# Kernel tuning notes

Hardware: AMD Instinct MI355X
Metric: run time of the kernel (lower is better)

The kernel has to match this reference:

```python
import jax, jax.numpy as jnp
import numpy as np

N = 20000       # total atoms
E = 320000      # edges (avg degree 16)
F = 128         # num_features
R = 32          # num_radial
NB = 3          # num_blocks
CUTOFF = 5.0
MAX_Z = 37      # max_atomic_number + 1
MIN_DIST = 0.3
PI = 3.141592653589793


def swish(x):
    return x * jax.nn.sigmoid(x)


def sph_harm_l2(rhat):
    # Real spherical harmonics lmax=2, e3nn ordering, 'component' normalization.
    x, y, z = rhat[:, 0], rhat[:, 1], rhat[:, 2]
    s3, s5, s15 = 1.7320508075688772, 2.23606797749979, 3.872983346207417
    sh1 = jnp.stack([s3 * y, s3 * z, s3 * x], axis=-1)                    # l=1 (odd)
    sh2 = jnp.stack([s15 * x * y, s15 * y * z, 0.5 * s5 * (3.0 * z * z - 1.0),
                     s15 * z * x, 0.5 * s15 * (x * x - y * y)], axis=-1)  # l=2 (even)
    return sh1, sh2


def setup_inputs() -> dict:
    key = jax.random.key(0)
    ks = jax.random.split(key, 16)
    rn = lambda k, shape, scale: jax.random.normal(k, shape, dtype=jnp.float32) * scale
    inp = {}
    inp["z"] = jax.random.randint(ks[0], (N,), 0, MAX_Z)
    inp["pos"] = rn(ks[1], (N, 3), 3.0)
    inp["edge_index"] = jax.random.randint(ks[2], (2, E), 0, N)
    # embedding params
    inp["emb_table"] = rn(ks[3], (MAX_Z, F), 1.0)
    inp["emb_W"] = rn(ks[4], (F, F), F ** -0.5)
    inp["emb_b"] = jnp.zeros((F,), jnp.float32)
    # trainable Bessel frequencies (init n*pi, as in bessel RBF)
    inp["bessel_freq"] = jnp.arange(1, R + 1, dtype=jnp.float32) * PI
    # per-block params, stacked over NB blocks
    inp["Wf1"] = rn(ks[5], (NB, R, F), R ** -0.5)
    inp["bf1"] = jnp.zeros((NB, F), jnp.float32)
    inp["Wf2"] = rn(ks[6], (NB, F, 4 * F), F ** -0.5)
    inp["Wsrc"] = rn(ks[7], (NB, F, F), F ** -0.5)
    inp["Wu"] = rn(ks[8], (NB, F, 3 * F), F ** -0.5)
    inp["W1o"] = rn(ks[9], (NB, F, F), F ** -0.5)
    inp["W1e"] = rn(ks[10], (NB, F, F), F ** -0.5)
    inp["W2e"] = rn(ks[11], (NB, F, F), F ** -0.5)
    inp["Wup"] = rn(ks[12], (NB, 4 * F, F), (4 * F) ** -0.5)
    return inp


def forward(z, pos, edge_index, emb_table, emb_W, emb_b, bessel_freq,
            Wf1, bf1, Wf2, Wsrc, Wu, W1o, W1e, W2e, Wup):
    i, j = edge_index[0], edge_index[1]
    rij = pos[j] - pos[i]                                   # [E,3]
    r = jnp.sqrt(jnp.sum(rij * rij, axis=-1) + 1e-12)       # [E]
    rhat = rij / (r[:, None] + 1e-6)
    # mask replaces the edge filtering (min_distance and radius cutoff)
    edge_mask = ((r >= MIN_DIST) & (r < CUTOFF)).astype(pos.dtype)
    sh1, sh2 = sph_harm_l2(rhat)                            # [E,3], [E,5]
    # trainable Bessel RBF with cosine cutoff envelope
    fc = 0.5 * (jnp.cos(PI * r / CUTOFF) + 1.0) * edge_mask
    rbf = jnp.sqrt(2.0 / CUTOFF) * jnp.sin(bessel_freq[None, :] * r[:, None] / CUTOFF) / (r[:, None] + 1e-6)
    rbf = rbf * fc[:, None]                                 # [E,R]
    # atom embedding
    S = swish(emb_table[z] @ emb_W + emb_b)                 # [N,F]
    T = jnp.zeros((N, 11, F), S.dtype)                      # 1o(3)+1e(3)+2e(5) x F channels
    for b in range(NB):
        # radial filter network -> per-edge gates
        w = swish(rbf @ Wf1[b] + bf1[b]) @ Wf2[b]           # [E,4F]
        w = w * edge_mask[:, None]
        wS, w1, w2, w3 = jnp.split(w, 4, axis=-1)
        Sj = S[j]                                           # [E,F] gather
        # scalar messages
        mS = wS * swish(Sj @ Wsrc[b])                       # [E,F]
        aggS = jax.ops.segment_sum(mS, i, num_segments=N)   # [N,F]
        # equivariant messages: sh(l) outer-product edge features
        u1, u2, u3 = jnp.split(Sj @ Wu[b], 3, axis=-1)
        m1o = sh1[:, :, None] * (w1 * u1)[:, None, :]       # [E,3,F]
        m1e = sh1[:, :, None] * (w2 * u2)[:, None, :]       # [E,3,F]
        m2e = sh2[:, :, None] * (w3 * u3)[:, None, :]       # [E,5,F]
        mT = jnp.concatenate([m1o, m1e, m2e], axis=1)       # [E,11,F]
        aggT = jax.ops.segment_sum(mT, i, num_segments=N)   # [N,11,F] scatter-add
        Tin = T + aggT
        # per-irrep channel mixing (self-interaction)
        T1o = jnp.einsum('nmf,fg->nmg', Tin[:, 0:3], W1o[b])
        T1e = jnp.einsum('nmf,fg->nmg', Tin[:, 3:6], W1e[b])
        T2e = jnp.einsum('nmf,fg->nmg', Tin[:, 6:11], W2e[b])
        T = jnp.concatenate([T1o, T1e, T2e], axis=1)
        # invariant norms of each irrep feed back into scalar track
        inv = jnp.concatenate([jnp.sum(T1o * T1o, 1), jnp.sum(T1e * T1e, 1),
                               jnp.sum(T2e * T2e, 1)], axis=-1)   # [N,3F]
        S = S + swish(jnp.concatenate([aggS, inv], axis=-1) @ Wup[b])
    return S, T.reshape(N, 11 * F)


def reference(z, pos, edge_index, emb_table, emb_W, emb_b, bessel_freq,
              Wf1, bf1, Wf2, Wsrc, Wu, W1o, W1e, W2e, Wup):
    return forward(z, pos, edge_index, emb_table, emb_W, emb_b, bessel_freq,
                   Wf1, bf1, Wf2, Wsrc, Wu, W1o, W1e, W2e, Wup)
```

## Files before the change

kernel.cpp:

```cpp
#include <hip/hip_runtime.h>
#include <cstdint>
#include <cstddef>

#define NN 20000
#define EE 320000
#define FF 128
#define RR 32
#define MTE 16

typedef float  f32x4  __attribute__((ext_vector_type(4)));
typedef short  bf16x8 __attribute__((ext_vector_type(8)));

__device__ __forceinline__ float swishf(float x) {
    return x / (1.f + __expf(-x));
}
__device__ __forceinline__ unsigned short f2bf(float f) {
    unsigned int u = __builtin_bit_cast(unsigned int, f);
    u = (u + 0x7FFFu + ((u >> 16) & 1u)) >> 16;
    return (unsigned short)u;
}
__device__ __forceinline__ float bf2f(unsigned short h) {
    unsigned int u = ((unsigned int)h) << 16;
    return __builtin_bit_cast(float, u);
}

__global__ __launch_bounds__(256) void geom_deg_kernel(
    const float* __restrict__ pos, const int* __restrict__ eidx,
    int* __restrict__ deg)
{
    int e = blockIdx.x * 256 + threadIdx.x;
    if (e >= EE) return;
    int i = eidx[e], j = eidx[EE + e];
    float dx = pos[3*j+0] - pos[3*i+0];
    float dy = pos[3*j+1] - pos[3*i+1];
    float dz = pos[3*j+2] - pos[3*i+2];
    float r = sqrtf(dx*dx + dy*dy + dz*dz + 1e-12f);
    if (r >= 0.3f && r < 5.0f) atomicAdd(&deg[i], 1);
}

__global__ __launch_bounds__(256) void scan_kernel(
    const int* __restrict__ deg, int* __restrict__ cursor, int* __restrict__ cnt)
{
    __shared__ int part[256];
    const int t = threadIdx.x;
    const int lo = t * 79;
    const int hi = min(lo + 79, NN);
    int s = 0;
    for (int k = lo; k < hi; k++) s += deg[k];
    part[t] = s;
    __syncthreads();
    for (int off = 1; off < 256; off <<= 1) {
        int v = (t >= off) ? part[t - off] : 0;
        __syncthreads();
        part[t] += v;
        __syncthreads();
    }
    int run = (t == 0) ? 0 : part[t - 1];
    for (int k = lo; k < hi; k++) { cursor[k] = run; run += deg[k]; }
    if (t == 255) cnt[0] = part[255];
}

__global__ __launch_bounds__(256) void geom_scatter_kernel(
    const float* __restrict__ pos, const int* __restrict__ eidx,
    const float* __restrict__ freq, int* __restrict__ cursor,
    int* __restrict__ ei, int* __restrict__ ej,
    float* __restrict__ sh, unsigned short* __restrict__ rbfq)
{
    int e = blockIdx.x * 256 + threadIdx.x;
    if (e >= EE) return;
    int i = eidx[e], j = eidx[EE + e];
    float dx = pos[3*j+0] - pos[3*i+0];
    float dy = pos[3*j+1] - pos[3*i+1];
    float dz = pos[3*j+2] - pos[3*i+2];
    float r = sqrtf(dx*dx + dy*dy + dz*dz + 1e-12f);
    if (!(r >= 0.3f && r < 5.0f)) return;
    int slot = atomicAdd(&cursor[i], 1);
    ei[slot] = i; ej[slot] = j;
    float ir = 1.f / (r + 1e-6f);
    float x = dx*ir, y = dy*ir, z = dz*ir;
    const float s3 = 1.7320508075688772f, s5 = 2.23606797749979f, s15 = 3.872983346207417f;
    float* shp = sh + (size_t)slot * 8;
    shp[0] = s3*y; shp[1] = s3*z; shp[2] = s3*x;
    shp[3] = s15*x*y; shp[4] = s15*y*z; shp[5] = 0.5f*s5*(3.f*z*z - 1.f);
    shp[6] = s15*z*x; shp[7] = 0.5f*s15*(x*x - y*y);
    float fc = 0.5f * (cosf(3.14159265358979323846f * r * 0.2f) + 1.f);
    float pref = 0.6324555320336759f * fc * ir;
    unsigned short* rp = rbfq + (size_t)slot * RR;
    for (int k = 0; k < RR; k++) rp[k] = f2bf(pref * sinf(freq[k] * r * 0.2f));
}

__global__ __launch_bounds__(128) void embed_kernel(
    const int* __restrict__ z, const float* __restrict__ emb_table,
    const float* __restrict__ emb_W, const float* __restrict__ emb_b,
    float* __restrict__ S)
{
    int n = blockIdx.x;
    int f = threadIdx.x;
    __shared__ float row[FF];
    row[f] = emb_table[(size_t)z[n]*FF + f];
    __syncthreads();
    float acc = emb_b[f];
    for (int k = 0; k < FF; k++) acc += row[k] * emb_W[k*FF + f];
    S[(size_t)n*FF + f] = swishf(acc);
}

__global__ __launch_bounds__(256) void pack_kernel(
    const float* __restrict__ W1o, const float* __restrict__ W1e,
    const float* __restrict__ W2e, const float* __restrict__ Wup,
    unsigned short* __restrict__ ph, unsigned short* __restrict__ pl)
{
    int t = blockIdx.x * 256 + threadIdx.x;
    if (t >= 3 * 14336) return;
    int b = t / 14336, r = t % 14336;
    const float* src; int nks; size_t dstoff;
    if (r < 6144) {
        int mat = r / 2048, rr = r % 2048;
        src = (mat == 0 ? W1o : mat == 1 ? W1e : W2e) + (size_t)b * 16384;
        nks = 4;
        dstoff = (size_t)b * 114688 + (size_t)mat * 16384 + (size_t)rr * 8;
        r = rr;
    } else {
        int rr = r - 6144;
        src = Wup + (size_t)b * 65536;
        nks = 16;
        dstoff = (size_t)b * 114688 + 49152 + (size_t)rr * 8;
        r = rr;
    }
    int lane = r & 63;
    int fi = r >> 6;
    int ks = fi % nks, ct = fi / nks;
    int col = ct * 16 + (lane & 15);
    int kb = ks * 32 + (lane >> 4) * 8;
    #pragma unroll
    for (int e = 0; e < 8; e++) {
        float v = src[(size_t)(kb + e) * 128 + col];
        unsigned short h = f2bf(v);
        ph[dstoff + e] = h;
        pl[dstoff + e] = f2bf(v - bf2f(h));
    }
}

__global__ __launch_bounds__(256) void pack_pu_kernel(
    const float* __restrict__ Wsrc, const float* __restrict__ Wu,
    unsigned short* __restrict__ packPU)
{
    int t = blockIdx.x * 256 + threadIdx.x;
    if (t >= 3 * 8192) return;
    int b = t / 8192, r = t % 8192;
    int lane = r & 63, fi = r >> 6;
    int ks = fi & 3, ct = fi >> 2;
    int kb = ks * 32 + (lane >> 4) * 8;
    int colq = lane & 15;
    const float* src; int col, stride;
    if (ct < 8) { src = Wsrc + (size_t)b * 16384; col = ct*16 + colq; stride = 128; }
    else        { src = Wu   + (size_t)b * 49152; col = (ct-8)*16 + colq; stride = 384; }
    size_t dst = (size_t)b * 65536 + (size_t)fi * 512 + (size_t)lane * 8;
    #pragma unroll
    for (int e = 0; e < 8; e++)
        packPU[dst + e] = f2bf(src[(size_t)(kb + e) * stride + col]);
}

__global__ __launch_bounds__(256) void pack_f2_kernel(
    const float* __restrict__ Wf2, unsigned short* __restrict__ packF2)
{
    int t = blockIdx.x * 256 + threadIdx.x;
    if (t >= 3 * 8192) return;
    int b = t / 8192, r = t % 8192;
    int lane = r & 63, fi = r >> 6;
    int ks = fi & 3, ct = fi >> 2;
    int kb = ks * 32 + (lane >> 4) * 8;
    int col = ct * 16 + (lane & 15);
    const float* src = Wf2 + (size_t)b * 65536;
    size_t dst = (size_t)b * 65536 + (size_t)fi * 512 + (size_t)lane * 8;
    #pragma unroll
    for (int e = 0; e < 8; e++)
        packF2[dst + e] = f2bf(src[(size_t)(kb + e) * 512 + col]);
}

__global__ __launch_bounds__(256) void proj_kernel(
    const float* __restrict__ S, const unsigned short* __restrict__ packPU,
    unsigned short* __restrict__ PU)
{
    __shared__ float stage[16][132];
    const int tid = threadIdx.x;
    const int n0 = blockIdx.x * 16;

    for (int idx = tid; idx < 512; idx += 256) {
        int row = idx >> 5, k4 = (idx & 31) << 2;
        *(float4*)&stage[row][k4] = *(const float4*)&S[((size_t)(n0 + row) << 7) + k4];
    }
    __syncthreads();

    const int lane = tid & 63;
    const int wid  = tid >> 6;
    const int row  = lane & 15;
    const int k0   = (lane >> 4) * 8;

    f32x4 acc[8];
    #pragma unroll
    for (int c = 0; c < 8; c++) acc[c] = (f32x4){0.f, 0.f, 0.f, 0.f};

    #pragma unroll
    for (int ks = 0; ks < 4; ks++) {
        const float* sp = &stage[row][ks*32 + k0];
        bf16x8 a;
        #pragma unroll
        for (int e = 0; e < 8; e++) a[e] = (short)f2bf(sp[e]);
        #pragma unroll
        for (int cti = 0; cti < 8; cti++) {
            int ct = wid * 8 + cti;
            bf16x8 b = *(const bf16x8*)(packPU + (((size_t)ct * 4 + ks) * 64 + lane) * 8);
            acc[cti] = __builtin_amdgcn_mfma_f32_16x16x32_bf16(a, b, acc[cti], 0, 0, 0);
        }
    }

    #pragma unroll
    for (int cti = 0; cti < 8; cti++) {
        int ct = wid * 8 + cti;
        int col = ct * 16 + (lane & 15);
        #pragma unroll
        for (int q = 0; q < 4; q++) {
            int n = n0 + (lane >> 4) * 4 + q;
            float v = acc[cti][q];
            if (ct < 8) v = swishf(v);
            PU[(size_t)n * 512 + col] = f2bf(v);
        }
    }
}

__global__ __launch_bounds__(256) void msg_kernel(
    const int* __restrict__ cnt,
    const int* __restrict__ ei, const int* __restrict__ ej,
    const float* __restrict__ sh, const unsigned short* __restrict__ rbfq,
    const float* __restrict__ Wf1, const float* __restrict__ bf1,
    const unsigned short* __restrict__ packF2, const unsigned short* __restrict__ PU,
    float* __restrict__ aggS, float* __restrict__ aggT)
{
    const int Ea = cnt[0];
    const int base = blockIdx.x * MTE;
    if (base >= Ea) return;
    const int nval = min(MTE, Ea - base);
    const int tid = threadIdx.x;

    __shared__ float          rbf_s[MTE][RR];
    __shared__ unsigned short h_s[MTE][FF];
    __shared__ unsigned short w_s[MTE][512];
    __shared__ float          sh_s[MTE][8];
    __shared__ int            i_s[MTE];
    __shared__ int            j_s[MTE];

    if (tid < MTE) {
        i_s[tid] = (tid < nval) ? ei[base + tid] : -1;
        j_s[tid] = (tid < nval) ? ej[base + tid] : 0;
    }
    if (tid >= 64 && tid < 64 + MTE*8) {
        int t = tid - 64, e = t >> 3;
        sh_s[e][t & 7] = (e < nval) ? sh[(size_t)(base + e)*8 + (t & 7)] : 0.f;
    }
    for (int t = tid; t < MTE*RR; t += 256) {
        int e = t >> 5, k = t & 31;
        rbf_s[e][k] = (e < nval) ? bf2f(rbfq[(size_t)(base + e)*RR + k]) : 0.f;
    }
    __syncthreads();

    {
        const int f = tid & 127, eh = tid >> 7;
        float hacc[8];
        float bb = bf1[f];
        #pragma unroll
        for (int k = 0; k < 8; k++) hacc[k] = bb;
        for (int r = 0; r < RR; r++) {
            float wv = Wf1[r*FF + f];
            #pragma unroll
            for (int k = 0; k < 8; k++) hacc[k] += rbf_s[eh*8 + k][r] * wv;
        }
        #pragma unroll
        for (int k = 0; k < 8; k++) h_s[eh*8 + k][f] = f2bf(swishf(hacc[k]));
    }
    __syncthreads();

    {
        const int lane = tid & 63;
        const int wid  = tid >> 6;
        const int ra   = lane & 15;
        const int k0   = (lane >> 4) * 8;
        f32x4 acc[8];
        #pragma unroll
        for (int c = 0; c < 8; c++) acc[c] = (f32x4){0.f, 0.f, 0.f, 0.f};
        #pragma unroll
        for (int ks = 0; ks < 4; ks++) {
            bf16x8 a = *(const bf16x8*)&h_s[ra][ks*32 + k0];
            #pragma unroll
            for (int cti = 0; cti < 8; cti++) {
                int ct = wid * 8 + cti;
                bf16x8 b = *(const bf16x8*)(packF2 + (((size_t)ct * 4 + ks) * 64 + lane) * 8);
                acc[cti] = __builtin_amdgcn_mfma_f32_16x16x32_bf16(a, b, acc[cti], 0, 0, 0);
            }
        }
        #pragma unroll
        for (int cti = 0; cti < 8; cti++) {
            int ct = wid * 8 + cti;
            int col = ct * 16 + (lane & 15);
            #pragma unroll
            for (int q = 0; q < 4; q++)
                w_s[(lane >> 4)*4 + q][col] = f2bf(acc[cti][q]);
        }
    }
    __syncthreads();

    const int f = tid & 127;
    if (tid < 128) {
        float aS = 0.f, a3 = 0.f, a4 = 0.f, a5 = 0.f;
        int cur = i_s[0];
        for (int e = 0; e < nval; e++) {
            int ie = i_s[e];
            if (ie != cur) {
                atomicAdd(&aggS[((size_t)cur << 7) + f], aS);
                size_t bT = (((size_t)cur*11 + 3) << 7) + f;
                atomicAdd(&aggT[bT], a3); atomicAdd(&aggT[bT + 128], a4); atomicAdd(&aggT[bT + 256], a5);
                aS = a3 = a4 = a5 = 0.f; cur = ie;
            }
            const unsigned short* pu = PU + (size_t)j_s[e] * 512;
            float wS = bf2f(w_s[e][f]),       P  = bf2f(pu[f]);
            float w2 = bf2f(w_s[e][256 + f]), U2 = bf2f(pu[256 + f]);
            aS += wS * P;
            float v = w2 * U2;
            a3 += sh_s[e][0]*v; a4 += sh_s[e][1]*v; a5 += sh_s[e][2]*v;
        }
        atomicAdd(&aggS[((size_t)cur << 7) + f], aS);
        size_t bT = (((size_t)cur*11 + 3) << 7) + f;
        atomicAdd(&aggT[bT], a3); atomicAdd(&aggT[bT + 128], a4); atomicAdd(&aggT[bT + 256], a5);
    } else {
        float a0 = 0.f, a1 = 0.f, a2 = 0.f;
        float a6 = 0.f, a7 = 0.f, a8 = 0.f, a9 = 0.f, a10 = 0.f;
        int cur = i_s[0];
        for (int e = 0; e < nval; e++) {
            int ie = i_s[e];
            if (ie != cur) {
                size_t bT = (((size_t)cur*11) << 7) + f;
                atomicAdd(&aggT[bT], a0); atomicAdd(&aggT[bT + 128], a1); atomicAdd(&aggT[bT + 256], a2);
                size_t bT2 = (((size_t)cur*11 + 6) << 7) + f;
                atomicAdd(&aggT[bT2], a6); atomicAdd(&aggT[bT2 + 128], a7); atomicAdd(&aggT[bT2 + 256], a8);
                atomicAdd(&aggT[bT2 + 384], a9); atomicAdd(&aggT[bT2 + 512], a10);
                a0 = a1 = a2 = a6 = a7 = a8 = a9 = a10 = 0.f; cur = ie;
            }
            const unsigned short* pu = PU + (size_t)j_s[e] * 512;
            float w1 = bf2f(w_s[e][128 + f]), U1 = bf2f(pu[128 + f]);
            float w3 = bf2f(w_s[e][384 + f]), U3 = bf2f(pu[384 + f]);
            float v1 = w1 * U1;
            a0 += sh_s[e][0]*v1; a1 += sh_s[e][1]*v1; a2 += sh_s[e][2]*v1;
            float v3 = w3 * U3;
            a6 += sh_s[e][3]*v3; a7 += sh_s[e][4]*v3; a8 += sh_s[e][5]*v3;
            a9 += sh_s[e][6]*v3; a10 += sh_s[e][7]*v3;
        }
        size_t bT = (((size_t)cur*11) << 7) + f;
        atomicAdd(&aggT[bT], a0); atomicAdd(&aggT[bT + 128], a1); atomicAdd(&aggT[bT + 256], a2);
        size_t bT2 = (((size_t)cur*11 + 6) << 7) + f;
        atomicAdd(&aggT[bT2], a6); atomicAdd(&aggT[bT2 + 128], a7); atomicAdd(&aggT[bT2 + 256], a8);
        atomicAdd(&aggT[bT2 + 384], a9); atomicAdd(&aggT[bT2 + 512], a10);
    }
}

template<int GSIZE>
__global__ __launch_bounds__(256) void tgemm_kernel(
    const float* __restrict__ aggT,
    const unsigned short* __restrict__ Wh, const unsigned short* __restrict__ Wl,
    float* __restrict__ T, float* __restrict__ inv,
    int goff, int invoff, int addT)
{
    __shared__ float stage[GSIZE][16][132];
    const int tid = threadIdx.x;
    const int n0 = blockIdx.x * 16;

    const int total = GSIZE * 16 * 32;
    for (int idx = tid; idx < total; idx += 256) {
        int mg  = idx >> 9;
        int rem = idx & 511;
        int row = rem >> 5;
        int k4  = (rem & 31) << 2;
        size_t g = (((size_t)(n0 + row) * 11 + goff + mg) << 7) + k4;
        float4 v = *(const float4*)&aggT[g];
        if (addT) {
            float4 tv = *(const float4*)&T[g];
            v.x += tv.x; v.y += tv.y; v.z += tv.z; v.w += tv.w;
        }
        *(float4*)&stage[mg][row][k4] = v;
    }
    __syncthreads();

    const int lane = tid & 63;
    const int wid  = tid >> 6;
    const int row  = lane & 15;
    const int k0   = (lane >> 4) * 8;

    f32x4 acc[GSIZE][2];
    #pragma unroll
    for (int mg = 0; mg < GSIZE; mg++) {
        acc[mg][0] = (f32x4){0.f, 0.f, 0.f, 0.f};
        acc[mg][1] = (f32x4){0.f, 0.f, 0.f, 0.f};
    }

    #pragma unroll
    for (int ks = 0; ks < 4; ks++) {
        bf16x8 ah[GSIZE], al[GSIZE];
        #pragma unroll
        for (int mg = 0; mg < GSIZE; mg++) {
            const float* sp = &stage[mg][row][ks*32 + k0];
            float v0[4], v1[4];
            *(float4*)v0 = *(const float4*)sp;
            *(float4*)v1 = *(const float4*)(sp + 4);
            #pragma unroll
            for (int e = 0; e < 4; e++) {
                unsigned short h0 = f2bf(v0[e]);
                ah[mg][e]   = (short)h0;
                al[mg][e]   = (short)f2bf(v0[e] - bf2f(h0));
                unsigned short h1 = f2bf(v1[e]);
                ah[mg][4+e] = (short)h1;
                al[mg][4+e] = (short)f2bf(v1[e] - bf2f(h1));
            }
        }
        #pragma unroll
        for (int cti = 0; cti < 2; cti++) {
            const int ct = wid * 2 + cti;
            size_t boff = (((size_t)ct * 4 + ks) * 64 + lane) * 8;
            bf16x8 bh = *(const bf16x8*)(Wh + boff);
            bf16x8 bl = *(const bf16x8*)(Wl + boff);
            #pragma unroll
            for (int mg = 0; mg < GSIZE; mg++) {
                acc[mg][cti] = __builtin_amdgcn_mfma_f32_16x16x32_bf16(ah[mg], bh, acc[mg][cti], 0, 0, 0);
                acc[mg][cti] = __builtin_amdgcn_mfma_f32_16x16x32_bf16(al[mg], bh, acc[mg][cti], 0, 0, 0);
                acc[mg][cti] = __builtin_amdgcn_mfma_f32_16x16x32_bf16(ah[mg], bl, acc[mg][cti], 0, 0, 0);
            }
        }
    }

    #pragma unroll
    for (int cti = 0; cti < 2; cti++) {
        const int ct = wid * 2 + cti;
        const int fc = ct * 16 + (lane & 15);
        #pragma unroll
        for (int q = 0; q < 4; q++) {
            const int n = n0 + (lane >> 4) * 4 + q;
            float iv = 0.f;
            #pragma unroll
            for (int mg = 0; mg < GSIZE; mg++) {
                float o = acc[mg][cti][q];
                T[(((size_t)n * 11 + goff + mg) << 7) + fc] = o;
                iv += o * o;
            }
            inv[(size_t)n * 384 + invoff + fc] = iv;
        }
    }
}

__global__ __launch_bounds__(256) void sgemm2_kernel(
    const float* __restrict__ aggS, const float* __restrict__ inv,
    const unsigned short* __restrict__ Wh, const unsigned short* __restrict__ Wl,
    float* __restrict__ S)
{
    __shared__ float stage[16][516];
    const int tid = threadIdx.x;
    const int n0 = blockIdx.x * 16;

    for (int idx = tid; idx < 16 * 128; idx += 256) {
        int row = idx >> 7;
        int k4  = (idx & 127) << 2;
        float4 v;
        if (k4 < 128) v = *(const float4*)&aggS[((size_t)(n0 + row) << 7) + k4];
        else          v = *(const float4*)&inv[(size_t)(n0 + row) * 384 + (k4 - 128)];
        *(float4*)&stage[row][k4] = v;
    }
    __syncthreads();

    const int lane = tid & 63;
    const int wid  = tid >> 6;
    const int row  = lane & 15;
    const int k0   = (lane >> 4) * 8;

    f32x4 acc[2];
    acc[0] = (f32x4){0.f, 0.f, 0.f, 0.f};
    acc[1] = (f32x4){0.f, 0.f, 0.f, 0.f};

    for (int ks = 0; ks < 16; ks++) {
        const float* sp = &stage[row][ks*32 + k0];
        float v0[4], v1[4];
        *(float4*)v0 = *(const float4*)sp;
        *(float4*)v1 = *(const float4*)(sp + 4);
        bf16x8 ah, al;
        #pragma unroll
        for (int e = 0; e < 4; e++) {
            unsigned short h0 = f2bf(v0[e]);
            ah[e]   = (short)h0;
            al[e]   = (short)f2bf(v0[e] - bf2f(h0));
            unsigned short h1 = f2bf(v1[e]);
            ah[4+e] = (short)h1;
            al[4+e] = (short)f2bf(v1[e] - bf2f(h1));
        }
        #pragma unroll
        for (int cti = 0; cti < 2; cti++) {
            const int ct = wid * 2 + cti;
            size_t boff = (((size_t)ct * 16 + ks) * 64 + lane) * 8;
            bf16x8 bh = *(const bf16x8*)(Wh + boff);
            bf16x8 bl = *(const bf16x8*)(Wl + boff);
            acc[cti] = __builtin_amdgcn_mfma_f32_16x16x32_bf16(ah, bh, acc[cti], 0, 0, 0);
            acc[cti] = __builtin_amdgcn_mfma_f32_16x16x32_bf16(al, bh, acc[cti], 0, 0, 0);
            acc[cti] = __builtin_amdgcn_mfma_f32_16x16x32_bf16(ah, bl, acc[cti], 0, 0, 0);
        }
    }

    #pragma unroll
    for (int cti = 0; cti < 2; cti++) {
        const int ct = wid * 2 + cti;
        const int fc = ct * 16 + (lane & 15);
        #pragma unroll
        for (int q = 0; q < 4; q++) {
            const int n = n0 + (lane >> 4) * 4 + q;
            size_t o = ((size_t)n << 7) + fc;
            S[o] += swishf(acc[cti][q]);
        }
    }
}

extern "C" void kernel_launch(void* const* d_in, const int* in_sizes, int n_in,
                              void* d_out, int out_size, void* d_ws, size_t ws_size,
                              hipStream_t stream)
{
    const int*   z         = (const int*)  d_in[0];
    const float* pos       = (const float*)d_in[1];
    const int*   eidx      = (const int*)  d_in[2];
    const float* emb_table = (const float*)d_in[3];
    const float* emb_W     = (const float*)d_in[4];
    const float* emb_b     = (const float*)d_in[5];
    const float* freq      = (const float*)d_in[6];
    const float* Wf1       = (const float*)d_in[7];
    const float* bf1       = (const float*)d_in[8];
    const float* Wf2       = (const float*)d_in[9];
    const float* Wsrc      = (const float*)d_in[10];
    const float* Wu        = (const float*)d_in[11];
    const float* W1o       = (const float*)d_in[12];
    const float* W1e       = (const float*)d_in[13];
    const float* W2e       = (const float*)d_in[14];
    const float* Wup       = (const float*)d_in[15];

    float* S = (float*)d_out;
    float* T = S + (size_t)NN*FF;

    char* w = (char*)d_ws;
    int*   cnt    = (int*)w;                      w += 256;
    int*   deg    = (int*)w;                      w += (size_t)NN*4 + 128;
    int*   cursor = (int*)w;                      w += (size_t)NN*4 + 128;
    int*   ei     = (int*)w;                      w += (size_t)EE*4;
    int*   ej     = (int*)w;                      w += (size_t)EE*4;
    float* sh     = (float*)w;                    w += (size_t)EE*8*4;
    unsigned short* rbfq = (unsigned short*)w;    w += (size_t)EE*RR*2;
    unsigned short* PU   = (unsigned short*)w;    w += (size_t)NN*512*2;
    float* aggS   = (float*)w;                    w += (size_t)NN*FF*4;
    float* aggT   = (float*)w;                    w += (size_t)NN*11*FF*4;
    float* inv    = (float*)w;                    w += (size_t)NN*384*4;
    unsigned short* packH  = (unsigned short*)w;  w += (size_t)344064*2;
    unsigned short* packL  = (unsigned short*)w;  w += (size_t)344064*2;
    unsigned short* packPU = (unsigned short*)w;  w += (size_t)3*65536*2;
    unsigned short* packF2 = (unsigned short*)w;  w += (size_t)3*65536*2;

    hipMemsetAsync(deg, 0, (size_t)NN*4, stream);

    geom_deg_kernel<<<(EE + 255)/256, 256, 0, stream>>>(pos, eidx, deg);
    scan_kernel<<<1, 256, 0, stream>>>(deg, cursor, cnt);
    geom_scatter_kernel<<<(EE + 255)/256, 256, 0, stream>>>(pos, eidx, freq, cursor, ei, ej, sh, rbfq);
    embed_kernel<<<NN, 128, 0, stream>>>(z, emb_table, emb_W, emb_b, S);
    pack_kernel<<<(3*14336 + 255)/256, 256, 0, stream>>>(W1o, W1e, W2e, Wup, packH, packL);
    pack_pu_kernel<<<(3*8192 + 255)/256, 256, 0, stream>>>(Wsrc, Wu, packPU);
    pack_f2_kernel<<<(3*8192 + 255)/256, 256, 0, stream>>>(Wf2, packF2);

    for (int b = 0; b < 3; b++) {
        hipMemsetAsync(aggS, 0, (size_t)NN*FF*4 + (size_t)NN*11*FF*4, stream);
        proj_kernel<<<NN/16, 256, 0, stream>>>(S, packPU + (size_t)b*65536, PU);
        msg_kernel<<<(EE + MTE - 1)/MTE, 256, 0, stream>>>(
            cnt, ei, ej, sh, rbfq,
            Wf1 + (size_t)b*RR*FF, bf1 + (size_t)b*FF,
            packF2 + (size_t)b*65536, PU, aggS, aggT);

        const unsigned short* H = packH + (size_t)b*114688;
        const unsigned short* L = packL + (size_t)b*114688;
        tgemm_kernel<3><<<NN/16, 256, 0, stream>>>(aggT, H +     0, L +     0, T, inv, 0,   0, b > 0);
        tgemm_kernel<3><<<NN/16, 256, 0, stream>>>(aggT, H + 16384, L + 16384, T, inv, 3, 128, b > 0);
        tgemm_kernel<5><<<NN/16, 256, 0, stream>>>(aggT, H + 32768, L + 32768, T, inv, 6, 256, b > 0);
        sgemm2_kernel<<<NN/16, 256, 0, stream>>>(aggS, inv, H + 49152, L + 49152, S);
    }
}
```

Measured before the change: 985.2 us.

## Fuse message passing, aggregation and node GEMMs into one per-node-block kernel

Replaces the per-layer message kernel, global atomic aggregation, memset and four node GEMM kernels with a single kernel. Each block owns 8 destination nodes, walks their CSR edge range, and accumulates messages in LDS without atomics. It then applies the T and S channel-mixing GEMMs directly from LDS. PU and the per-edge filter weights are interleaved so one 8-byte load fetches all four channels per feature. This drops the global aggT/aggS/inv round-trips and the atomics, but the 16-row MFMA tiles now carry only 8 valid rows, and degree imbalance between blocks may cause load imbalance.

Result: slower. 2.164 ms (+119.6%).

```diff
diff --git a/kernel.cpp b/kernel.cpp
--- a/kernel.cpp
+++ b/kernel.cpp
@@ -6,7 +6,7 @@
 #define EE 320000
 #define FF 128
 #define RR 32
-#define MTE 16
+#define NB_NODES 8
 
 typedef float  f32x4  __attribute__((ext_vector_type(4)));
 typedef short  bf16x8 __attribute__((ext_vector_type(8)));
@@ -39,7 +39,7 @@
 }
 
 __global__ __launch_bounds__(256) void scan_kernel(
-    const int* __restrict__ deg, int* __restrict__ cursor, int* __restrict__ cnt)
+    const int* __restrict__ deg, int* __restrict__ cursor, int* __restrict__ cstart)
 {
     __shared__ int part[256];
     const int t = threadIdx.x;
@@ -56,8 +56,8 @@
         __syncthreads();
     }
     int run = (t == 0) ? 0 : part[t - 1];
-    for (int k = lo; k < hi; k++) { cursor[k] = run; run += deg[k]; }
-    if (t == 255) cnt[0] = part[255];
+    for (int k = lo; k < hi; k++) { cursor[k] = run; cstart[k] = run; run += deg[k]; }
+    if (t == 255) cstart[NN] = run;
 }
 
 __global__ __launch_bounds__(256) void geom_scatter_kernel(
@@ -217,306 +217,308 @@
     #pragma unroll
     for (int cti = 0; cti < 8; cti++) {
         int ct = wid * 8 + cti;
-        int col = ct * 16 + (lane & 15);
+        int cblk = ct >> 3;
+        int fcol = (ct & 7) * 16 + (lane & 15);
         #pragma unroll
         for (int q = 0; q < 4; q++) {
             int n = n0 + (lane >> 4) * 4 + q;
             float v = acc[cti][q];
-            if (ct < 8) v = swishf(v);
-            PU[(size_t)n * 512 + col] = f2bf(v);
-        }
-    }
-}
-
-__global__ __launch_bounds__(256) void msg_kernel(
-    const int* __restrict__ cnt,
+            if (cblk == 0) v = swishf(v);
+            PU[(size_t)n * 512 + fcol * 4 + cblk] = f2bf(v);
+        }
+    }
+}
+
+template<int GS>
+__device__ __forceinline__ void tgemm_group(
+    const float* aggT_lds, float* inv_lds,
+    const unsigned short* __restrict__ Hb, const unsigned short* __restrict__ Lb,
+    float* __restrict__ T, int n0, int goff, int invoff, int lane, int wid)
+{
+    const int arow = lane & 15;
+    const int k0 = (lane >> 4) * 8;
+    f32x4 acc[GS][2];
+    #pragma unroll
+    for (int mg = 0; mg < GS; mg++) {
+        acc[mg][0] = (f32x4){0.f, 0.f, 0.f, 0.f};
+        acc[mg][1] = (f32x4){0.f, 0.f, 0.f, 0.f};
+    }
+    #pragma unroll
+    for (int ks = 0; ks < 4; ks++) {
+        bf16x8 ah[GS], al[GS];
+        #pragma unroll
+        for (int mg = 0; mg < GS; mg++) {
+            float v[8];
+            if (arow < NB_NODES) {
+                const float* sp = aggT_lds + arow*1452 + (goff+mg)*132 + ks*32 + k0;
+                *(float4*)&v[0] = *(const float4*)sp;
+                *(float4*)&v[4] = *(const float4*)(sp + 4);
+            } else {
+                #pragma unroll
+                for (int e = 0; e < 8; e++) v[e] = 0.f;
+            }
+            #pragma unroll
+            for (int e = 0; e < 8; e++) {
+                unsigned short h = f2bf(v[e]);
+                ah[mg][e] = (short)h;
+                al[mg][e] = (short)f2bf(v[e] - bf2f(h));
+            }
+        }
+        #pragma unroll
+        for (int cti = 0; cti < 2; cti++) {
+            int ct = wid * 2 + cti;
+            size_t boff = (((size_t)ct * 4 + ks) * 64 + lane) * 8;
+            bf16x8 bh = *(const bf16x8*)(Hb + boff);
+            bf16x8 bl = *(const bf16x8*)(Lb + boff);
+            #pragma unroll
+            for (int mg = 0; mg < GS; mg++) {
+                acc[mg][cti] = __builtin_amdgcn_mfma_f32_16x16x32_bf16(ah[mg], bh, acc[mg][cti], 0, 0, 0);
+                acc[mg][cti] = __builtin_amdgcn_mfma_f32_16x16x32_bf16(al[mg], bh, acc[mg][cti], 0, 0, 0);
+                acc[mg][cti] = __builtin_amdgcn_mfma_f32_16x16x32_bf16(ah[mg], bl, acc[mg][cti], 0, 0, 0);
+            }
+        }
+    }
+    #pragma unroll
+    for (int cti = 0; cti < 2; cti++) {
+        int ct = wid * 2 + cti;
+        int fc = ct * 16 + (lane & 15);
+        #pragma unroll
+        for (int q = 0; q < 4; q++) {
+            int rowD = (lane >> 4) * 4 + q;
+            if (rowD < NB_NODES) {
+                float iv = 0.f;
+                #pragma unroll
+                for (int mg = 0; mg < GS; mg++) {
+                    float o = acc[mg][cti][q];
+                    T[(((size_t)(n0+rowD)*11 + goff + mg) << 7) + fc] = o;
+                    iv += o * o;
+                }
+                inv_lds[rowD*388 + invoff + fc] = iv;
+            }
+        }
+    }
+}
+
+__global__ __launch_bounds__(256, 2) void fused_layer_kernel(
+    const int* __restrict__ cstart,
     const int* __restrict__ ei, const int* __restrict__ ej,
     const float* __restrict__ sh, const unsigned short* __restrict__ rbfq,
     const float* __restrict__ Wf1, const float* __restrict__ bf1,
     const unsigned short* __restrict__ packF2, const unsigned short* __restrict__ PU,
-    float* __restrict__ aggS, float* __restrict__ aggT)
-{
-    const int Ea = cnt[0];
-    const int base = blockIdx.x * MTE;
-    if (base >= Ea) return;
-    const int nval = min(MTE, Ea - base);
+    const unsigned short* __restrict__ packH, const unsigned short* __restrict__ packL,
+    float* __restrict__ S, float* __restrict__ T, int addT)
+{
+    __shared__ float aggT_lds[NB_NODES * 1452];
+    __shared__ float aggS_lds[NB_NODES * 132];
+    __shared__ unsigned short upool[16 * 520];
+    __shared__ unsigned short h_s[16][128];
+    __shared__ float rbf_s[16][32];
+    __shared__ float sh_s[16][8];
+    __shared__ int   i_s[16], j_s[16];
+
     const int tid = threadIdx.x;
-
-    __shared__ float          rbf_s[MTE][RR];
-    __shared__ unsigned short h_s[MTE][FF];
-    __shared__ unsigned short w_s[MTE][512];
-    __shared__ float          sh_s[MTE][8];
-    __shared__ int            i_s[MTE];
-    __shared__ int            j_s[MTE];
-
-    if (tid < MTE) {
-        i_s[tid] = (tid < nval) ? ei[base + tid] : -1;
-        j_s[tid] = (tid < nval) ? ej[base + tid] : 0;
-    }
-    if (tid >= 64 && tid < 64 + MTE*8) {
-        int t = tid - 64, e = t >> 3;
-        sh_s[e][t & 7] = (e < nval) ? sh[(size_t)(base + e)*8 + (t & 7)] : 0.f;
-    }
-    for (int t = tid; t < MTE*RR; t += 256) {
-        int e = t >> 5, k = t & 31;
-        rbf_s[e][k] = (e < nval) ? bf2f(rbfq[(size_t)(base + e)*RR + k]) : 0.f;
-    }
-    __syncthreads();
-
-    {
-        const int f = tid & 127, eh = tid >> 7;
-        float hacc[8];
-        float bb = bf1[f];
-        #pragma unroll
-        for (int k = 0; k < 8; k++) hacc[k] = bb;
-        for (int r = 0; r < RR; r++) {
-            float wv = Wf1[r*FF + f];
-            #pragma unroll
-            for (int k = 0; k < 8; k++) hacc[k] += rbf_s[eh*8 + k][r] * wv;
-        }
-        #pragma unroll
-        for (int k = 0; k < 8; k++) h_s[eh*8 + k][f] = f2bf(swishf(hacc[k]));
-    }
-    __syncthreads();
-
-    {
-        const int lane = tid & 63;
-        const int wid  = tid >> 6;
-        const int ra   = lane & 15;
-        const int k0   = (lane >> 4) * 8;
-        f32x4 acc[8];
-        #pragma unroll
-        for (int c = 0; c < 8; c++) acc[c] = (f32x4){0.f, 0.f, 0.f, 0.f};
-        #pragma unroll
-        for (int ks = 0; ks < 4; ks++) {
-            bf16x8 a = *(const bf16x8*)&h_s[ra][ks*32 + k0];
+    const int n0 = blockIdx.x * NB_NODES;
+    const int estart = cstart[n0];
+    const int eend   = cstart[n0 + NB_NODES];
+    const int f    = tid & 127;
+    const int half = tid >> 7;
+    const int lane = tid & 63;
+    const int wid  = tid >> 6;
+
+    for (int k = tid; k < NB_NODES*1452; k += 256) aggT_lds[k] = 0.f;
+    for (int k = tid; k < NB_NODES*132; k += 256)  aggS_lds[k] = 0.f;
+
+    float aS=0.f, a3=0.f, a4=0.f, a5=0.f;
+    float a0=0.f,a1=0.f,a2=0.f,a6=0.f,a7=0.f,a8=0.f,a9=0.f,a10=0.f;
+    int cur = -1;
+
+    for (int eoff = estart; eoff < eend; eoff += 16) {
+        const int te = min(16, eend - eoff);
+        __syncthreads();
+        if (tid < 16) {
+            i_s[tid] = (tid < te) ? ei[eoff + tid] : -1;
+            j_s[tid] = (tid < te) ? ej[eoff + tid] : 0;
+        }
+        if (tid >= 64 && tid < 192) {
+            int t = tid - 64, e = t >> 3;
+            sh_s[e][t & 7] = (e < te) ? sh[(size_t)(eoff + e)*8 + (t & 7)] : 0.f;
+        }
+        for (int t = tid; t < 512; t += 256) {
+            int e = t >> 5, k = t & 31;
+            rbf_s[e][k] = (e < te) ? bf2f(rbfq[(size_t)(eoff + e)*RR + k]) : 0.f;
+        }
+        __syncthreads();
+        if (cur < 0) cur = i_s[0];
+
+        uint2 puv[16];
+        #pragma unroll
+        for (int e = 0; e < 16; e++)
+            puv[e] = *(const uint2*)(PU + ((size_t)j_s[e] << 9) + (f << 2));
+
+        {
+            float hacc[8];
+            float bb = bf1[f];
+            #pragma unroll
+            for (int k = 0; k < 8; k++) hacc[k] = bb;
+            for (int r = 0; r < RR; r++) {
+                float wv = Wf1[r*FF + f];
+                #pragma unroll
+                for (int k = 0; k < 8; k++) hacc[k] += rbf_s[half*8 + k][r] * wv;
+            }
+            #pragma unroll
+            for (int k = 0; k < 8; k++)
+                h_s[half*8 + k][f] = (half*8 + k < te) ? f2bf(swishf(hacc[k])) : 0;
+        }
+        __syncthreads();
+
+        {
+            const int ra = lane & 15, k0 = (lane >> 4) * 8;
+            f32x4 wacc[8];
+            #pragma unroll
+            for (int c = 0; c < 8; c++) wacc[c] = (f32x4){0.f, 0.f, 0.f, 0.f};
+            #pragma unroll
+            for (int ks = 0; ks < 4; ks++) {
+                bf16x8 a = *(const bf16x8*)&h_s[ra][ks*32 + k0];
+                #pragma unroll
+                for (int cti = 0; cti < 8; cti++) {
+                    int ct = wid * 8 + cti;
+                    bf16x8 b = *(const bf16x8*)(packF2 + (((size_t)ct * 4 + ks) * 64 + lane) * 8);
+                    wacc[cti] = __builtin_amdgcn_mfma_f32_16x16x32_bf16(a, b, wacc[cti], 0, 0, 0);
+                }
+            }
             #pragma unroll
             for (int cti = 0; cti < 8; cti++) {
                 int ct = wid * 8 + cti;
-                bf16x8 b = *(const bf16x8*)(packF2 + (((size_t)ct * 4 + ks) * 64 + lane) * 8);
-                acc[cti] = __builtin_amdgcn_mfma_f32_16x16x32_bf16(a, b, acc[cti], 0, 0, 0);
-            }
-        }
-        #pragma unroll
-        for (int cti = 0; cti < 8; cti++) {
-            int ct = wid * 8 + cti;
-            int col = ct * 16 + (lane & 15);
-            #pragma unroll
-            for (int q = 0; q < 4; q++)
-                w_s[(lane >> 4)*4 + q][col] = f2bf(acc[cti][q]);
+                int cblk = ct >> 3;
+                int fcol = (ct & 7) * 16 + (lane & 15);
+                #pragma unroll
+                for (int q = 0; q < 4; q++)
+                    upool[((lane >> 4)*4 + q)*520 + fcol*4 + cblk] = f2bf(wacc[cti][q]);
+            }
+        }
+        __syncthreads();
+
+        #pragma unroll
+        for (int e = 0; e < 16; e++) {
+            bool valid = (e < te);
+            int ie = valid ? i_s[e] : cur;
+            if (ie != cur) {
+                int ln = cur - n0;
+                float* base = aggT_lds + ln*1452;
+                if (half == 0) {
+                    aggS_lds[ln*132 + f] = aS;
+                    base[3*132+f] = a3; base[4*132+f] = a4; base[5*132+f] = a5;
+                    aS = a3 = a4 = a5 = 0.f;
+                } else {
+                    base[f] = a0; base[132+f] = a1; base[264+f] = a2;
+                    base[6*132+f] = a6; base[7*132+f] = a7; base[8*132+f] = a8;
+                    base[9*132+f] = a9; base[10*132+f] = a10;
+                    a0=a1=a2=a6=a7=a8=a9=a10=0.f;
+                }
+                cur = ie;
+            }
+            uint2 wv2 = *(const uint2*)&upool[e*520 + f*4];
+            uint2 pv  = puv[e];
+            if (half == 0) {
+                float wS = bf2f((unsigned short)(wv2.x & 0xffff));
+                float w2 = bf2f((unsigned short)(wv2.y & 0xffff));
+                float P  = bf2f((unsigned short)(pv.x  & 0xffff));
+                float U2 = bf2f((unsigned short)(pv.y  & 0xffff));
+                aS += wS * P;
+                float v = w2 * U2;
+                a3 += sh_s[e][0]*v; a4 += sh_s[e][1]*v; a5 += sh_s[e][2]*v;
+            } else {
+                float w1 = bf2f((unsigned short)(wv2.x >> 16));
+                float w3 = bf2f((unsigned short)(wv2.y >> 16));
+                float U1 = bf2f((unsigned short)(pv.x  >> 16));
+                float U3 = bf2f((unsigned short)(pv.y  >> 16));
+                float v1 = w1 * U1;
+                a0 += sh_s[e][0]*v1; a1 += sh_s[e][1]*v1; a2 += sh_s[e][2]*v1;
+                float v3 = w3 * U3;
+                a6 += sh_s[e][3]*v3; a7 += sh_s[e][4]*v3; a8 += sh_s[e][5]*v3;
+                a9 += sh_s[e][6]*v3; a10 += sh_s[e][7]*v3;
+            }
+        }
+    }
+    if (eend > estart) {
+        int ln = cur - n0;
+        float* base = aggT_lds + ln*1452;
+        if (half == 0) {
+            aggS_lds[ln*132 + f] = aS;
+            base[3*132+f] = a3; base[4*132+f] = a4; base[5*132+f] = a5;
+        } else {
+            base[f] = a0; base[132+f] = a1; base[264+f] = a2;
+            base[6*132+f] = a6; base[7*132+f] = a7; base[8*132+f] = a8;
+            base[9*132+f] = a9; base[10*132+f] = a10;
         }
     }
     __syncthreads();
 
-    const int f = tid & 127;
-    if (tid < 128) {
-        float aS = 0.f, a3 = 0.f, a4 = 0.f, a5 = 0.f;
-        int cur = i_s[0];
-        for (int e = 0; e < nval; e++) {
-            int ie = i_s[e];
-            if (ie != cur) {
-                atomicAdd(&aggS[((size_t)cur << 7) + f], aS);
-                size_t bT = (((size_t)cur*11 + 3) << 7) + f;
-                atomicAdd(&aggT[bT], a3); atomicAdd(&aggT[bT + 128], a4); atomicAdd(&aggT[bT + 256], a5);
-                aS = a3 = a4 = a5 = 0.f; cur = ie;
-            }
-            const unsigned short* pu = PU + (size_t)j_s[e] * 512;
-            float wS = bf2f(w_s[e][f]),       P  = bf2f(pu[f]);
-            float w2 = bf2f(w_s[e][256 + f]), U2 = bf2f(pu[256 + f]);
-            aS += wS * P;
-            float v = w2 * U2;
-            a3 += sh_s[e][0]*v; a4 += sh_s[e][1]*v; a5 += sh_s[e][2]*v;
-        }
-        atomicAdd(&aggS[((size_t)cur << 7) + f], aS);
-        size_t bT = (((size_t)cur*11 + 3) << 7) + f;
-        atomicAdd(&aggT[bT], a3); atomicAdd(&aggT[bT + 128], a4); atomicAdd(&aggT[bT + 256], a5);
-    } else {
-        float a0 = 0.f, a1 = 0.f, a2 = 0.f;
-        float a6 = 0.f, a7 = 0.f, a8 = 0.f, a9 = 0.f, a10 = 0.f;
-        int cur = i_s[0];
-        for (int e = 0; e < nval; e++) {
-            int ie = i_s[e];
-            if (ie != cur) {
-                size_t bT = (((size_t)cur*11) << 7) + f;
-                atomicAdd(&aggT[bT], a0); atomicAdd(&aggT[bT + 128], a1); atomicAdd(&aggT[bT + 256], a2);
-                size_t bT2 = (((size_t)cur*11 + 6) << 7) + f;
-                atomicAdd(&aggT[bT2], a6); atomicAdd(&aggT[bT2 + 128], a7); atomicAdd(&aggT[bT2 + 256], a8);
-                atomicAdd(&aggT[bT2 + 384], a9); atomicAdd(&aggT[bT2 + 512], a10);
-                a0 = a1 = a2 = a6 = a7 = a8 = a9 = a10 = 0.f; cur = ie;
-            }
-            const unsigned short* pu = PU + (size_t)j_s[e] * 512;
-            float w1 = bf2f(w_s[e][128 + f]), U1 = bf2f(pu[128 + f]);
-            float w3 = bf2f(w_s[e][384 + f]), U3 = bf2f(pu[384 + f]);
-            float v1 = w1 * U1;
-            a0 += sh_s[e][0]*v1; a1 += sh_s[e][1]*v1; a2 += sh_s[e][2]*v1;
-            float v3 = w3 * U3;
-            a6 += sh_s[e][3]*v3; a7 += sh_s[e][4]*v3; a8 += sh_s[e][5]*v3;
-            a9 += sh_s[e][6]*v3; a10 += sh_s[e][7]*v3;
-        }
-        size_t bT = (((size_t)cur*11) << 7) + f;
-        atomicAdd(&aggT[bT], a0); atomicAdd(&aggT[bT + 128], a1); atomicAdd(&aggT[bT + 256], a2);
-        size_t bT2 = (((size_t)cur*11 + 6) << 7) + f;
-        atomicAdd(&aggT[bT2], a6); atomicAdd(&aggT[bT2 + 128], a7); atomicAdd(&aggT[bT2 + 256], a8);
-        atomicAdd(&aggT[bT2 + 384], a9); atomicAdd(&aggT[bT2 + 512], a10);
-    }
-}
-
-template<int GSIZE>
-__global__ __launch_bounds__(256) void tgemm_kernel(
-    const float* __restrict__ aggT,
-    const unsigned short* __restrict__ Wh, const unsigned short* __restrict__ Wl,
-    float* __restrict__ T, float* __restrict__ inv,
-    int goff, int invoff, int addT)
-{
-    __shared__ float stage[GSIZE][16][132];
-    const int tid = threadIdx.x;
-    const int n0 = blockIdx.x * 16;
-
-    const int total = GSIZE * 16 * 32;
-    for (int idx = tid; idx < total; idx += 256) {
-        int mg  = idx >> 9;
-        int rem = idx & 511;
-        int row = rem >> 5;
-        int k4  = (rem & 31) << 2;
-        size_t g = (((size_t)(n0 + row) * 11 + goff + mg) << 7) + k4;
-        float4 v = *(const float4*)&aggT[g];
-        if (addT) {
-            float4 tv = *(const float4*)&T[g];
-            v.x += tv.x; v.y += tv.y; v.z += tv.z; v.w += tv.w;
-        }
-        *(float4*)&stage[mg][row][k4] = v;
+    if (addT) {
+        for (int idx = tid; idx < NB_NODES*11*32; idx += 256) {
+            int node = idx / 352;
+            int rem  = idx % 352;
+            int m = rem >> 5, k4 = (rem & 31) << 2;
+            float4 tv = *(const float4*)&T[(((size_t)(n0 + node)*11 + m) << 7) + k4];
+            float* dst = &aggT_lds[node*1452 + m*132 + k4];
+            dst[0] += tv.x; dst[1] += tv.y; dst[2] += tv.z; dst[3] += tv.w;
+        }
     }
     __syncthreads();
 
-    const int lane = tid & 63;
-    const int wid  = tid >> 6;
-    const int row  = lane & 15;
-    const int k0   = (lane >> 4) * 8;
-
-    f32x4 acc[GSIZE][2];
-    #pragma unroll
-    for (int mg = 0; mg < GSIZE; mg++) {
-        acc[mg][0] = (f32x4){0.f, 0.f, 0.f, 0.f};
-        acc[mg][1] = (f32x4){0.f, 0.f, 0.f, 0.f};
-    }
-
-    #pragma unroll
-    for (int ks = 0; ks < 4; ks++) {
-        bf16x8 ah[GSIZE], al[GSIZE];
-        #pragma unroll
-        for (int mg = 0; mg < GSIZE; mg++) {
-            const float* sp = &stage[mg][row][ks*32 + k0];
-            float v0[4], v1[4];
-            *(float4*)v0 = *(const float4*)sp;
-            *(float4*)v1 = *(const float4*)(sp + 4);
-            #pragma unroll
-            for (int e = 0; e < 4; e++) {
-                unsigned short h0 = f2bf(v0[e]);
-                ah[mg][e]   = (short)h0;
-                al[mg][e]   = (short)f2bf(v0[e] - bf2f(h0));
-                unsigned short h1 = f2bf(v1[e]);
-                ah[mg][4+e] = (short)h1;
-                al[mg][4+e] = (short)f2bf(v1[e] - bf2f(h1));
+    float* inv_lds = (float*)upool;
+    tgemm_group<3>(aggT_lds, inv_lds, packH +     0, packL +     0, T, n0, 0,   0, lane, wid);
+    tgemm_group<3>(aggT_lds, inv_lds, packH + 16384, packL + 16384, T, n0, 3, 128, lane, wid);
+    tgemm_group<5>(aggT_lds, inv_lds, packH + 32768, packL + 32768, T, n0, 6, 256, lane, wid);
+    __syncthreads();
+
+    {
+        const int arow = lane & 15;
+        const int k0 = (lane >> 4) * 8;
+        f32x4 acc[2];
+        acc[0] = (f32x4){0.f, 0.f, 0.f, 0.f};
+        acc[1] = (f32x4){0.f, 0.f, 0.f, 0.f};
+        #pragma unroll
+        for (int ks = 0; ks < 16; ks++) {
+            float v[8];
+            #pragma unroll
+            for (int e = 0; e < 8; e++) {
+                int kk = ks*32 + k0 + e;
+                float x = 0.f;
+                if (arow < NB_NODES)
+                    x = (kk < 128) ? aggS_lds[arow*132 + kk] : inv_lds[arow*388 + (kk - 128)];
+                v[e] = x;
+            }
+            bf16x8 ah, al;
+            #pragma unroll
+            for (int e = 0; e < 8; e++) {
+                unsigned short h = f2bf(v[e]);
+                ah[e] = (short)h;
+                al[e] = (short)f2bf(v[e] - bf2f(h));
+            }
+            #pragma unroll
+            for (int cti = 0; cti < 2; cti++) {
+                int ct = wid * 2 + cti;
+                size_t boff = (((size_t)ct * 16 + ks) * 64 + lane) * 8 + 49152;
+                bf16x8 bh = *(const bf16x8*)(packH + boff);
+                bf16x8 bl = *(const bf16x8*)(packL + boff);
+                acc[cti] = __builtin_amdgcn_mfma_f32_16x16x32_bf16(ah, bh, acc[cti], 0, 0, 0);
+                acc[cti] = __builtin_amdgcn_mfma_f32_16x16x32_bf16(al, bh, acc[cti], 0, 0, 0);
+                acc[cti] = __builtin_amdgcn_mfma_f32_16x16x32_bf16(ah, bl, acc[cti], 0, 0, 0);
             }
         }
         #pragma unroll
         for (int cti = 0; cti < 2; cti++) {
-            const int ct = wid * 2 + cti;
-            size_t boff = (((size_t)ct * 4 + ks) * 64 + lane) * 8;
-            bf16x8 bh = *(const bf16x8*)(Wh + boff);
-            bf16x8 bl = *(const bf16x8*)(Wl + boff);
-            #pragma unroll
-            for (int mg = 0; mg < GSIZE; mg++) {
-                acc[mg][cti] = __builtin_amdgcn_mfma_f32_16x16x32_bf16(ah[mg], bh, acc[mg][cti], 0, 0, 0);
-                acc[mg][cti] = __builtin_amdgcn_mfma_f32_16x16x32_bf16(al[mg], bh, acc[mg][cti], 0, 0, 0);
-                acc[mg][cti] = __builtin_amdgcn_mfma_f32_16x16x32_bf16(ah[mg], bl, acc[mg][cti], 0, 0, 0);
-            }
-        }
-    }
-
-    #pragma unroll
-    for (int cti = 0; cti < 2; cti++) {
-        const int ct = wid * 2 + cti;
-        const int fc = ct * 16 + (lane & 15);
-        #pragma unroll
-        for (int q = 0; q < 4; q++) {
-            const int n = n0 + (lane >> 4) * 4 + q;
-            float iv = 0.f;
-            #pragma unroll
-            for (int mg = 0; mg < GSIZE; mg++) {
-                float o = acc[mg][cti][q];
-                T[(((size_t)n * 11 + goff + mg) << 7) + fc] = o;
-                iv += o * o;
-            }
-            inv[(size_t)n * 384 + invoff + fc] = iv;
-        }
-    }
-}
-
-__global__ __launch_bounds__(256) void sgemm2_kernel(
-    const float* __restrict__ aggS, const float* __restrict__ inv,
-    const unsigned short* __restrict__ Wh, const unsigned short* __restrict__ Wl,
-    float* __restrict__ S)
-{
-    __shared__ float stage[16][516];
-    const int tid = threadIdx.x;
-    const int n0 = blockIdx.x * 16;
-
-    for (int idx = tid; idx < 16 * 128; idx += 256) {
-        int row = idx >> 7;
-        int k4  = (idx & 127) << 2;
-        float4 v;
-        if (k4 < 128) v = *(const float4*)&aggS[((size_t)(n0 + row) << 7) + k4];
-        else          v = *(const float4*)&inv[(size_t)(n0 + row) * 384 + (k4 - 128)];
-        *(float4*)&stage[row][k4] = v;
-    }
-    __syncthreads();
-
-    const int lane = tid & 63;
-    const int wid  = tid >> 6;
-    const int row  = lane & 15;
-    const int k0   = (lane >> 4) * 8;
-
-    f32x4 acc[2];
-    acc[0] = (f32x4){0.f, 0.f, 0.f, 0.f};
-    acc[1] = (f32x4){0.f, 0.f, 0.f, 0.f};
-
-    for (int ks = 0; ks < 16; ks++) {
-        const float* sp = &stage[row][ks*32 + k0];
-        float v0[4], v1[4];
-        *(float4*)v0 = *(const float4*)sp;
-        *(float4*)v1 = *(const float4*)(sp + 4);
-        bf16x8 ah, al;
-        #pragma unroll
-        for (int e = 0; e < 4; e++) {
-            unsigned short h0 = f2bf(v0[e]);
-            ah[e]   = (short)h0;
-            al[e]   = (short)f2bf(v0[e] - bf2f(h0));
-            unsigned short h1 = f2bf(v1[e]);
-            ah[4+e] = (short)h1;
-            al[4+e] = (short)f2bf(v1[e] - bf2f(h1));
-        }
-        #pragma unroll
-        for (int cti = 0; cti < 2; cti++) {
-            const int ct = wid * 2 + cti;
-            size_t boff = (((size_t)ct * 16 + ks) * 64 + lane) * 8;
-            bf16x8 bh = *(const bf16x8*)(Wh + boff);
-            bf16x8 bl = *(const bf16x8*)(Wl + boff);
-            acc[cti] = __builtin_amdgcn_mfma_f32_16x16x32_bf16(ah, bh, acc[cti], 0, 0, 0);
-            acc[cti] = __builtin_amdgcn_mfma_f32_16x16x32_bf16(al, bh, acc[cti], 0, 0, 0);
-            acc[cti] = __builtin_amdgcn_mfma_f32_16x16x32_bf16(ah, bl, acc[cti], 0, 0, 0);
-        }
-    }
-
-    #pragma unroll
-    for (int cti = 0; cti < 2; cti++) {
-        const int ct = wid * 2 + cti;
-        const int fc = ct * 16 + (lane & 15);
-        #pragma unroll
-        for (int q = 0; q < 4; q++) {
-            const int n = n0 + (lane >> 4) * 4 + q;
-            size_t o = ((size_t)n << 7) + fc;
-            S[o] += swishf(acc[cti][q]);
+            int ct = wid * 2 + cti;
+            int fc = ct * 16 + (lane & 15);
+            #pragma unroll
+            for (int q = 0; q < 4; q++) {
+                int rowD = (lane >> 4) * 4 + q;
+                if (rowD < NB_NODES) {
+                    size_t o = ((size_t)(n0 + rowD) << 7) + fc;
+                    S[o] += swishf(acc[cti][q]);
+                }
+            }
         }
     }
 }
@@ -546,17 +548,14 @@
     float* T = S + (size_t)NN*FF;
 
     char* w = (char*)d_ws;
-    int*   cnt    = (int*)w;                      w += 256;
     int*   deg    = (int*)w;                      w += (size_t)NN*4 + 128;
     int*   cursor = (int*)w;                      w += (size_t)NN*4 + 128;
+    int*   cstart = (int*)w;                      w += (size_t)(NN+1)*4 + 124;
     int*   ei     = (int*)w;                      w += (size_t)EE*4;
     int*   ej     = (int*)w;                      w += (size_t)EE*4;
     float* sh     = (float*)w;                    w += (size_t)EE*8*4;
     unsigned short* rbfq = (unsigned short*)w;    w += (size_t)EE*RR*2;
     unsigned short* PU   = (unsigned short*)w;    w += (size_t)NN*512*2;
-    float* aggS   = (float*)w;                    w += (size_t)NN*FF*4;
-    float* aggT   = (float*)w;                    w += (size_t)NN*11*FF*4;
-    float* inv    = (float*)w;                    w += (size_t)NN*384*4;
     unsigned short* packH  = (unsigned short*)w;  w += (size_t)344064*2;
     unsigned short* packL  = (unsigned short*)w;  w += (size_t)344064*2;
     unsigned short* packPU = (unsigned short*)w;  w += (size_t)3*65536*2;
@@ -565,7 +564,7 @@
     hipMemsetAsync(deg, 0, (size_t)NN*4, stream);
 
     geom_deg_kernel<<<(EE + 255)/256, 256, 0, stream>>>(pos, eidx, deg);
-    scan_kernel<<<1, 256, 0, stream>>>(deg, cursor, cnt);
+    scan_kernel<<<1, 256, 0, stream>>>(deg, cursor, cstart);
     geom_scatter_kernel<<<(EE + 255)/256, 256, 0, stream>>>(pos, eidx, freq, cursor, ei, ej, sh, rbfq);
     embed_kernel<<<NN, 128, 0, stream>>>(z, emb_table, emb_W, emb_b, S);
     pack_kernel<<<(3*14336 + 255)/256, 256, 0, stream>>>(W1o, W1e, W2e, Wup, packH, packL);
@@ -573,18 +572,12 @@
     pack_f2_kernel<<<(3*8192 + 255)/256, 256, 0, stream>>>(Wf2, packF2);
 
     for (int b = 0; b < 3; b++) {
-        hipMemsetAsync(aggS, 0, (size_t)NN*FF*4 + (size_t)NN*11*FF*4, stream);
         proj_kernel<<<NN/16, 256, 0, stream>>>(S, packPU + (size_t)b*65536, PU);
-        msg_kernel<<<(EE + MTE - 1)/MTE, 256, 0, stream>>>(
-            cnt, ei, ej, sh, rbfq,
+        fused_layer_kernel<<<NN/NB_NODES, 256, 0, stream>>>(
+            cstart, ei, ej, sh, rbfq,
             Wf1 + (size_t)b*RR*FF, bf1 + (size_t)b*FF,
-            packF2 + (size_t)b*65536, PU, aggS, aggT);
-
-        const unsigned short* H = packH + (size_t)b*114688;
-        const unsigned short* L = packL + (size_t)b*114688;
-        tgemm_kernel<3><<<NN/16, 256, 0, stream>>>(aggT, H +     0, L +     0, T, inv, 0,   0, b > 0);
-        tgemm_kernel<3><<<NN/16, 256, 0, stream>>>(aggT, H + 16384, L + 16384, T, inv, 3, 128, b > 0);
-        tgemm_kernel<5><<<NN/16, 256, 0, stream>>>(aggT, H + 32768, L + 32768, T, inv, 6, 256, b > 0);
-        sgemm2_kernel<<<NN/16, 256, 0, stream>>>(aggS, inv, H + 49152, L + 49152, S);
-    }
-}
+            packF2 + (size_t)b*65536, PU,
+            packH + (size_t)b*114688, packL + (size_t)b*114688,
+            S, T, b > 0);
+    }
+}
```
